# Kernel tuning notes

Measured on AMD Instinct MI355X. Metric: run time of the kernel, lower is better.

Reference implementation:

```python
import jax, jax.numpy as jnp
import numpy as np

D_IN = 1024
D_OUT = 1024
SEQ = 4096


def setup_inputs() -> dict:
    key = jax.random.key(0)
    kx, kq, kk, kv = jax.random.split(key, 4)
    x = jax.random.normal(kx, (SEQ, D_IN), dtype=jnp.float32)
    # original uses torch.rand (uniform [0,1)) for parameter init
    w_query = jax.random.uniform(kq, (D_IN, D_OUT), dtype=jnp.float32)
    w_key = jax.random.uniform(kk, (D_IN, D_OUT), dtype=jnp.float32)
    w_value = jax.random.uniform(kv, (D_IN, D_OUT), dtype=jnp.float32)
    return {"x": x, "w_query": w_query, "w_key": w_key, "w_value": w_value}


def reference(x, w_query, w_key, w_value):
    # QKV projections: [S, d_in] @ [d_in, d_out] -> [S, d_out]
    queries = x @ w_query
    keys = x @ w_key
    values = x @ w_value
    scale = keys.shape[-1] ** 0.5
    # full attention matrix [S, S]
    attn_scores = jnp.einsum('sd,td->st', queries, keys)
    attn_weights = jax.nn.softmax(attn_scores / scale, axis=-1)
    context_vecs = attn_weights @ values  # [S, d_out]
    return context_vecs
```

## Files before the change

kernel.cpp:

```cpp
#include <hip/hip_runtime.h>
#include <hip/hip_fp16.h>
#include <math.h>

#define SEQ    4096
#define DMODEL 1024

typedef _Float16 half8   __attribute__((ext_vector_type(8)));
typedef _Float16 half4v  __attribute__((ext_vector_type(4)));
typedef float    floatx4 __attribute__((ext_vector_type(4)));

__device__ inline void split_val(float v, _Float16& h, _Float16& l) {
    _Float16 hh = (_Float16)v;
    h = hh;
    l = (_Float16)(v - (float)hh);
}

__global__ __launch_bounds__(256) void prep(const float* __restrict__ x,
                                            const float* __restrict__ wq,
                                            const float* __restrict__ wk,
                                            const float* __restrict__ wv,
                                            _Float16* __restrict__ x_hi,
                                            _Float16* __restrict__ x_lo,
                                            _Float16* __restrict__ wqkT_hi,
                                            _Float16* __restrict__ wqkT_lo,
                                            _Float16* __restrict__ wvT) {
    __shared__ float tile[32][33];
    const int b = blockIdx.x;
    if (b < 3072) {
        const int which = b >> 10;
        const int bb = b & 1023;
        const int c0 = (bb & 31) * 32;
        const int r0 = (bb >> 5) * 32;
        const float* w = (which == 0) ? wq : (which == 1) ? wk : wv;
        const int tx = threadIdx.x & 31, ty = threadIdx.x >> 5;
#pragma unroll
        for (int j = 0; j < 4; ++j)
            tile[ty * 4 + j][tx] = w[(size_t)(r0 + ty * 4 + j) * DMODEL + c0 + tx];
        __syncthreads();
        if (which < 2) {
            _Float16* th = wqkT_hi + (size_t)which * DMODEL * DMODEL;
            _Float16* tl = wqkT_lo + (size_t)which * DMODEL * DMODEL;
#pragma unroll
            for (int j = 0; j < 4; ++j) {
                float v = tile[tx][ty * 4 + j];
                size_t idx = (size_t)(c0 + ty * 4 + j) * DMODEL + r0 + tx;
                _Float16 h, l;
                split_val(v, h, l);
                th[idx] = h;
                tl[idx] = l;
            }
        } else {
#pragma unroll
            for (int j = 0; j < 4; ++j)
                wvT[(size_t)(c0 + ty * 4 + j) * DMODEL + r0 + tx] =
                    (_Float16)tile[tx][ty * 4 + j];
        }
    } else {
        const int t0 = (b - 3072) * 256 + threadIdx.x;
#pragma unroll
        for (int rep = 0; rep < 4; ++rep) {
            const size_t i = (size_t)t0 + (size_t)rep * 262144;
            floatx4 v = *(const floatx4*)(x + 4 * i);
            half4v h, l;
#pragma unroll
            for (int j = 0; j < 4; ++j) {
                _Float16 hh = (_Float16)v[j];
                _Float16 ll = (_Float16)(v[j] - (float)hh);
                h[j] = hh;
                l[j] = ll;
            }
            *(half4v*)(x_hi + 4 * i) = h;
            *(half4v*)(x_lo + 4 * i) = l;
        }
    }
}

__global__ __launch_bounds__(512, 1) void gemm_qkproj_dp(
    const _Float16* __restrict__ Ahi, const _Float16* __restrict__ Alo,
    const _Float16* __restrict__ Bhi, const _Float16* __restrict__ Blo,
    _Float16* __restrict__ Qh, _Float16* __restrict__ Kh) {
    __shared__ _Float16 As[4][128][32];
    __shared__ _Float16 Bs[4][256][32];

    const int tid  = threadIdx.x;
    const int lane = tid & 63;
    const int wid  = tid >> 6;
    const int wm   = (wid >> 2) * 64;
    const int wn   = (wid & 3) * 64;

    const int rowA0 = blockIdx.y * 128;
    const int colB0 = blockIdx.x * 256;

    const int ar  = tid >> 2;
    const int ag  = tid & 3;
    const int ags = ag ^ ((ar >> 1) & 3);
    const char* aHiB = (const char*)(Ahi + (size_t)(rowA0 + ar) * DMODEL) + ags * 16;
    const char* aLoB = (const char*)(Alo + (size_t)(rowA0 + ar) * DMODEL) + ags * 16;
    const int br  = tid >> 2;
    const int bg  = tid & 3;
    const int bgs = bg ^ ((br >> 1) & 3);
    const char* bHi0 = (const char*)(Bhi + (size_t)(colB0 + br) * DMODEL) + bgs * 16;
    const char* bHi1 = (const char*)(Bhi + (size_t)(colB0 + br + 128) * DMODEL) + bgs * 16;
    const char* bLo0 = (const char*)(Blo + (size_t)(colB0 + br) * DMODEL) + bgs * 16;
    const char* bLo1 = (const char*)(Blo + (size_t)(colB0 + br + 128) * DMODEL) + bgs * 16;

#define STAGE_QA(tt)                                                                 \
    do {                                                                             \
        const int _s = (tt) & 3;                                                     \
        const char* _ab = ((tt) < 64) ? aHiB : aLoB;                                 \
        const size_t _ko = (size_t)((tt) & 31) * 64;                                 \
        __builtin_amdgcn_global_load_lds(                                            \
            (const __attribute__((address_space(1))) void*)(_ab + _ko),              \
            (__attribute__((address_space(3))) void*)&As[_s][ar][ag * 8], 16, 0, 0); \
    } while (0)

#define STAGE_QB(tt)                                                                 \
    do {                                                                             \
        const int _s = (tt) & 3;                                                     \
        const bool _lo = ((tt) >= 32) && ((tt) < 64);                                \
        const char* _b0 = _lo ? bLo0 : bHi0;                                         \
        const char* _b1 = _lo ? bLo1 : bHi1;                                         \
        const size_t _ko = (size_t)((tt) & 31) * 64;                                 \
        __builtin_amdgcn_global_load_lds(                                            \
            (const __attribute__((address_space(1))) void*)(_b0 + _ko),              \
            (__attribute__((address_space(3))) void*)&Bs[_s][br][bg * 8], 16, 0, 0); \
        __builtin_amdgcn_global_load_lds(                                            \
            (const __attribute__((address_space(1))) void*)(_b1 + _ko),              \
            (__attribute__((address_space(3))) void*)&Bs[_s][br + 128][bg * 8], 16, 0, 0);\
    } while (0)

    const int fm = lane & 15;
    const int fq = lane >> 4;
    const int ck = (fq ^ ((fm >> 1) & 3)) * 8;

    floatx4 acc[4][4] = {};

    auto tile_body = [&](int t, bool do_stage) {
        const int s = t & 3;
        half8 av[4], bv[4];
#pragma unroll
        for (int i = 0; i < 4; ++i) av[i] = *(const half8*)&As[s][wm + i * 16 + fm][ck];
#pragma unroll
        for (int j = 0; j < 4; ++j) bv[j] = *(const half8*)&Bs[s][wn + j * 16 + fm][ck];
        if (do_stage) { STAGE_QA(t + 3); STAGE_QB(t + 3); }
        asm volatile("" ::: "memory");
        __builtin_amdgcn_s_barrier();
        asm volatile("" ::: "memory");
        __builtin_amdgcn_s_setprio(1);
#pragma unroll
        for (int i = 0; i < 4; ++i)
#pragma unroll
            for (int j = 0; j < 4; ++j)
                acc[i][j] = __builtin_amdgcn_mfma_f32_16x16x32_f16(av[i], bv[j], acc[i][j], 0, 0, 0);
        __builtin_amdgcn_s_setprio(0);
    };

    STAGE_QA(0); STAGE_QB(0);
    STAGE_QA(1); STAGE_QB(1);
    STAGE_QA(2); STAGE_QB(2);
    asm volatile("s_waitcnt vmcnt(6)" ::: "memory");
    __builtin_amdgcn_s_barrier();
    asm volatile("" ::: "memory");

#pragma unroll 1
    for (int t = 0; t < 93; ++t) {
        tile_body(t, true);
        asm volatile("s_waitcnt vmcnt(6)" ::: "memory");
        __builtin_amdgcn_s_barrier();
        asm volatile("" ::: "memory");
    }
    tile_body(93, false);
    asm volatile("s_waitcnt vmcnt(3)" ::: "memory");
    __builtin_amdgcn_s_barrier();
    asm volatile("" ::: "memory");
    tile_body(94, false);
    asm volatile("s_waitcnt vmcnt(0)" ::: "memory");
    __builtin_amdgcn_s_barrier();
    asm volatile("" ::: "memory");
    tile_body(95, false);
#undef STAGE_QA
#undef STAGE_QB

    _Float16* dst = Qh;
    int cbase = colB0;
    if (colB0 >= 1024) { dst = Kh; cbase = colB0 - 1024; }

#pragma unroll
    for (int i = 0; i < 4; ++i) {
        const int growb = rowA0 + wm + i * 16 + fq * 4;
#pragma unroll
        for (int j = 0; j < 4; ++j) {
            const int gcol = wn + j * 16 + fm;
#pragma unroll
            for (int r = 0; r < 4; ++r)
                dst[(size_t)(growb + r) * DMODEL + cbase + gcol] =
                    (_Float16)acc[i][j][r];
        }
    }
}

__global__ __launch_bounds__(512, 2) void gemm_score_dp(
    const _Float16* __restrict__ Qh,
    const _Float16* __restrict__ Kh,
    _Float16* __restrict__ Ph, float* __restrict__ Marr, float* __restrict__ Larr,
    float scale) {
    __shared__ _Float16 As[4][256][32];
    __shared__ _Float16 Bs[4][256][32];

    const int tid  = threadIdx.x;
    const int lane = tid & 63;
    const int wid  = tid >> 6;
    const int wm   = (wid >> 2) * 128;
    const int wn   = (wid & 3) * 64;

    const int lin = blockIdx.y * 16 + blockIdx.x;
    const int swz = (lin & 7) * 32 + (lin >> 3);
    const int rowA0 = (swz >> 4) * 256;
    const int colB0 = (swz & 15) * 256;

    const int pr  = tid >> 2;
    const int pg  = tid & 3;
    const int pgs = pg ^ ((pr >> 1) & 3);

    const char* aSrc0 = (const char*)(Qh + (size_t)(rowA0 + pr) * DMODEL) + pgs * 16;
    const char* aSrc1 = (const char*)(Qh + (size_t)(rowA0 + pr + 128) * DMODEL) + pgs * 16;
    const char* bSrc0 = (const char*)(Kh + (size_t)(colB0 + pr) * DMODEL) + pgs * 16;
    const char* bSrc1 = (const char*)(Kh + (size_t)(colB0 + pr + 128) * DMODEL) + pgs * 16;

#define STAGE_A(t)                                                                  \
    do {                                                                            \
        const int _s = (t) & 3;                                                     \
        const size_t _ko = (size_t)(t) * 64;                                        \
        __builtin_amdgcn_global_load_lds(                                           \
            (const __attribute__((address_space(1))) void*)(aSrc0 + _ko),           \
            (__attribute__((address_space(3))) void*)&As[_s][pr][pg * 8], 16, 0, 0);\
        __builtin_amdgcn_global_load_lds(                                           \
            (const __attribute__((address_space(1))) void*)(aSrc1 + _ko),           \
            (__attribute__((address_space(3))) void*)&As[_s][pr + 128][pg * 8], 16, 0, 0);\
    } while (0)

#define STAGE_B(t)                                                                  \
    do {                                                                            \
        const int _s = (t) & 3;                                                     \
        const size_t _ko = (size_t)(t) * 64;                                        \
        __builtin_amdgcn_global_load_lds(                                           \
            (const __attribute__((address_space(1))) void*)(bSrc0 + _ko),           \
            (__attribute__((address_space(3))) void*)&Bs[_s][pr][pg * 8], 16, 0, 0);\
        __builtin_amdgcn_global_load_lds(                                           \
            (const __attribute__((address_space(1))) void*)(bSrc1 + _ko),           \
            (__attribute__((address_space(3))) void*)&Bs[_s][pr + 128][pg * 8], 16, 0, 0);\
    } while (0)

    const int fm = lane & 15;
    const int fq = lane >> 4;
    const int ck = (fq ^ ((fm >> 1) & 3)) * 8;

    floatx4 acc[8][4] = {};

    auto tile_body = [&](int t, bool do_stage) {
        const int s = t & 3;
        half8 av[4], av2[4], bv[4];
#pragma unroll
        for (int i = 0; i < 4; ++i) av[i]  = *(const half8*)&As[s][wm + i * 16 + fm][ck];
#pragma unroll
        for (int i = 0; i < 4; ++i) av2[i] = *(const half8*)&As[s][wm + 64 + i * 16 + fm][ck];
#pragma unroll
        for (int j = 0; j < 4; ++j) bv[j]  = *(const half8*)&Bs[s][wn + j * 16 + fm][ck];
        if (do_stage) { STAGE_A(t + 3); STAGE_B(t + 3); }
        asm volatile("" ::: "memory");
        __builtin_amdgcn_s_barrier();
        asm volatile("" ::: "memory");
        __builtin_amdgcn_s_setprio(1);
#pragma unroll
        for (int i = 0; i < 4; ++i)
#pragma unroll
            for (int j = 0; j < 4; ++j)
                acc[i][j] = __builtin_amdgcn_mfma_f32_16x16x32_f16(av[i], bv[j], acc[i][j], 0, 0, 0);
#pragma unroll
        for (int i = 0; i < 4; ++i)
#pragma unroll
            for (int j = 0; j < 4; ++j)
                acc[i + 4][j] = __builtin_amdgcn_mfma_f32_16x16x32_f16(av2[i], bv[j], acc[i + 4][j], 0, 0, 0);
        __builtin_amdgcn_s_setprio(0);
    };

    STAGE_A(0); STAGE_B(0);
    STAGE_A(1); STAGE_B(1);
    STAGE_A(2); STAGE_B(2);
    asm volatile("s_waitcnt vmcnt(8)" ::: "memory");
    __builtin_amdgcn_s_barrier();
    asm volatile("" ::: "memory");

#pragma unroll 1
    for (int t = 0; t < 29; ++t) {
        tile_body(t, true);
        asm volatile("s_waitcnt vmcnt(8)" ::: "memory");
        __builtin_amdgcn_s_barrier();
        asm volatile("" ::: "memory");
    }
    tile_body(29, false);
    asm volatile("s_waitcnt vmcnt(4)" ::: "memory");
    __builtin_amdgcn_s_barrier();
    asm volatile("" ::: "memory");
    tile_body(30, false);
    asm volatile("s_waitcnt vmcnt(0)" ::: "memory");
    __builtin_amdgcn_s_barrier();
    asm volatile("" ::: "memory");
    tile_body(31, false);
#undef STAGE_A
#undef STAGE_B

    const int tprime = (colB0 + wn) >> 6;
#pragma unroll
    for (int i = 0; i < 8; ++i) {
#pragma unroll
        for (int r = 0; r < 4; ++r) {
            const int grow = rowA0 + wm + i * 16 + fq * 4 + r;
            float s0 = acc[i][0][r] * scale;
            float s1 = acc[i][1][r] * scale;
            float s2 = acc[i][2][r] * scale;
            float s3 = acc[i][3][r] * scale;
            float mx = fmaxf(fmaxf(s0, s1), fmaxf(s2, s3));
            mx = fmaxf(mx, __shfl_xor(mx, 1));
            mx = fmaxf(mx, __shfl_xor(mx, 2));
            mx = fmaxf(mx, __shfl_xor(mx, 4));
            mx = fmaxf(mx, __shfl_xor(mx, 8));
            float p0 = __expf(s0 - mx);
            float p1 = __expf(s1 - mx);
            float p2 = __expf(s2 - mx);
            float p3 = __expf(s3 - mx);
            float sum = p0 + p1 + p2 + p3;
            sum += __shfl_xor(sum, 1);
            sum += __shfl_xor(sum, 2);
            sum += __shfl_xor(sum, 4);
            sum += __shfl_xor(sum, 8);
            _Float16* prow = Ph + (size_t)grow * SEQ + colB0 + wn + fm;
            prow[0]  = (_Float16)p0;
            prow[16] = (_Float16)p1;
            prow[32] = (_Float16)p2;
            prow[48] = (_Float16)p3;
            if (fm == 0) {
                Marr[(size_t)grow * 64 + tprime] = mx;
                Larr[(size_t)grow * 64 + tprime] = sum;
            }
        }
    }
}

__global__ __launch_bounds__(256) void compute_c(const float* __restrict__ Marr,
                                                 const float* __restrict__ Larr,
                                                 _Float16* __restrict__ CarrT) {
    __shared__ float c_s[64][65];
    const int row0 = blockIdx.x * 64;
    const int wv = threadIdx.x >> 6;
    const int ln = threadIdx.x & 63;

#pragma unroll
    for (int k = 0; k < 16; ++k) {
        const int r = wv * 16 + k;
        float mt = Marr[(size_t)(row0 + r) * 64 + ln];
        float lt = Larr[(size_t)(row0 + r) * 64 + ln];
        float m = mt;
#pragma unroll
        for (int off = 32; off > 0; off >>= 1) m = fmaxf(m, __shfl_xor(m, off));
        float e = __expf(mt - m);
        float L = lt * e;
#pragma unroll
        for (int off = 32; off > 0; off >>= 1) L += __shfl_xor(L, off);
        c_s[r][ln] = e / L;
    }
    __syncthreads();

#pragma unroll
    for (int k = 0; k < 16; ++k) {
        const int t = wv * 16 + k;
        CarrT[(size_t)t * SEQ + row0 + ln] = (_Float16)c_s[ln][t];
    }
}

__global__ __launch_bounds__(512, 1) void gemm_pv_dp(
    const _Float16* __restrict__ P,
    const _Float16* __restrict__ VT,
    const _Float16* __restrict__ CarrT,
    float* __restrict__ out) {
    __shared__ _Float16 As[4][128][64];
    __shared__ _Float16 Bs[4][128][64];
    __shared__ _Float16 cT[64][128];

    const int tid  = threadIdx.x;
    const int lane = tid & 63;
    const int wid  = tid >> 6;
    const int wm   = (wid >> 2) * 64;
    const int wn   = (wid & 3) * 32;

    const int rowA0 = blockIdx.y * 128;
    const int colB0 = blockIdx.x * 128;

    {
        int g = tid;
#pragma unroll
        for (int it = 0; it < 2; ++it, g += 512) {
            const int t  = g >> 4;
            const int r8 = (g & 15) * 8;
            *(half8*)&cT[t][r8] =
                *(const half8*)(CarrT + (size_t)t * SEQ + rowA0 + r8);
        }
    }
    __syncthreads();

    const int prow = tid >> 3;
    const int pgr  = tid & 7;
    const int ags  = pgr ^ (prow & 7);
    const char* aSrc0 = (const char*)(P  + (size_t)(rowA0 + prow) * SEQ) + ags * 16;
    const char* aSrc1 = (const char*)(P  + (size_t)(rowA0 + prow + 64) * SEQ) + ags * 16;
    const char* bSrc0 = (const char*)(VT + (size_t)(colB0 + prow) * SEQ) + ags * 16;
    const char* bSrc1 = (const char*)(VT + (size_t)(colB0 + prow + 64) * SEQ) + ags * 16;

#define STAGE_PA(tt)                                                                \
    do {                                                                            \
        const int _s = (tt) & 3;                                                    \
        const size_t _ko = (size_t)(tt) * 128;                                      \
        __builtin_amdgcn_global_load_lds(                                           \
            (const __attribute__((address_space(1))) void*)(aSrc0 + _ko),           \
            (__attribute__((address_space(3))) void*)&As[_s][prow][pgr * 8], 16, 0, 0);\
        __builtin_amdgcn_global_load_lds(                                           \
            (const __attribute__((address_space(1))) void*)(aSrc1 + _ko),           \
            (__attribute__((address_space(3))) void*)&As[_s][prow + 64][pgr * 8], 16, 0, 0);\
    } while (0)

#define STAGE_PB(tt)                                                                \
    do {                                                                            \
        const int _s = (tt) & 3;                                                    \
        const size_t _ko = (size_t)(tt) * 128;                                      \
        __builtin_amdgcn_global_load_lds(                                           \
            (const __attribute__((address_space(1))) void*)(bSrc0 + _ko),           \
            (__attribute__((address_space(3))) void*)&Bs[_s][prow][pgr * 8], 16, 0, 0);\
        __builtin_amdgcn_global_load_lds(                                           \
            (const __attribute__((address_space(1))) void*)(bSrc1 + _ko),           \
            (__attribute__((address_space(3))) void*)&Bs[_s][prow + 64][pgr * 8], 16, 0, 0);\
    } while (0)

    const int fm = lane & 15;
    const int fq = lane >> 4;
    const int ck0 = ((fq    ) ^ (fm & 7)) * 8;
    const int ck1 = ((fq + 4) ^ (fm & 7)) * 8;

    floatx4 acc[4][2] = {};

    auto tile_body = [&](int t, bool do_stage) {
        const int s = t & 3;
        half8 av[4], av2[4], bv[2], bv2[2];
        _Float16 cs[4];
#pragma unroll
        for (int i = 0; i < 4; ++i) {
            av[i]  = *(const half8*)&As[s][wm + i * 16 + fm][ck0];
            av2[i] = *(const half8*)&As[s][wm + i * 16 + fm][ck1];
            cs[i]  = cT[t][wm + i * 16 + fm];
        }
#pragma unroll
        for (int j = 0; j < 2; ++j) {
            bv[j]  = *(const half8*)&Bs[s][wn + j * 16 + fm][ck0];
            bv2[j] = *(const half8*)&Bs[s][wn + j * 16 + fm][ck1];
        }
#pragma unroll
        for (int i = 0; i < 4; ++i)
#pragma unroll
            for (int e = 0; e < 8; ++e) {
                av[i][e]  *= cs[i];
                av2[i][e] *= cs[i];
            }
        if (do_stage) { STAGE_PA(t + 3); STAGE_PB(t + 3); }
        asm volatile("" ::: "memory");
        __builtin_amdgcn_s_barrier();
        asm volatile("" ::: "memory");
        __builtin_amdgcn_s_setprio(1);
#pragma unroll
        for (int i = 0; i < 4; ++i)
#pragma unroll
            for (int j = 0; j < 2; ++j)
                acc[i][j] = __builtin_amdgcn_mfma_f32_16x16x32_f16(av[i], bv[j], acc[i][j], 0, 0, 0);
#pragma unroll
        for (int i = 0; i < 4; ++i)
#pragma unroll
            for (int j = 0; j < 2; ++j)
                acc[i][j] = __builtin_amdgcn_mfma_f32_16x16x32_f16(av2[i], bv2[j], acc[i][j], 0, 0, 0);
        __builtin_amdgcn_s_setprio(0);
    };

    STAGE_PA(0); STAGE_PB(0);
    STAGE_PA(1); STAGE_PB(1);
    STAGE_PA(2); STAGE_PB(2);
    asm volatile("s_waitcnt vmcnt(8)" ::: "memory");
    __builtin_amdgcn_s_barrier();
    asm volatile("" ::: "memory");

#pragma unroll 1
    for (int t = 0; t < 61; ++t) {
        tile_body(t, true);
        asm volatile("s_waitcnt vmcnt(8)" ::: "memory");
        __builtin_amdgcn_s_barrier();
        asm volatile("" ::: "memory");
    }
    tile_body(61, false);
    asm volatile("s_waitcnt vmcnt(4)" ::: "memory");
    __builtin_amdgcn_s_barrier();
    asm volatile("" ::: "memory");
    tile_body(62, false);
    asm volatile("s_waitcnt vmcnt(0)" ::: "memory");
    __builtin_amdgcn_s_barrier();
    asm volatile("" ::: "memory");
    tile_body(63, false);
#undef STAGE_PA
#undef STAGE_PB

#pragma unroll
    for (int i = 0; i < 4; ++i) {
        const int growb = rowA0 + wm + i * 16 + fq * 4;
#pragma unroll
        for (int j = 0; j < 2; ++j) {
            const int gcol = colB0 + wn + j * 16 + fm;
#pragma unroll
            for (int r = 0; r < 4; ++r)
                out[(size_t)(growb + r) * DMODEL + gcol] = acc[i][j][r];
        }
    }
}

template <int OUT_HALF>
__global__ __launch_bounds__(256) void gemm_h16_n64(
    const _Float16* __restrict__ A, int lda,
    const _Float16* __restrict__ B, int ldb,
    float* __restrict__ Cf, _Float16* __restrict__ Ch,
    int N, int K) {
    __shared__ _Float16 Ah[128][32];
    __shared__ _Float16 Bh[64][32];

    const int tid = threadIdx.x;
    const int lane = tid & 63;
    const int w = tid >> 6;
    const int wm = (w >> 1) * 64;
    const int wn = (w & 1) * 32;

    const int rowA0 = blockIdx.y * 128;
    const int colB0 = blockIdx.x * 64;

    const int sr = lane >> 2;
    const int sc = lane & 3;
    const int ra0 = w * 32 + sr;
    const int ra1 = ra0 + 16;
    const int rb0 = w * 16 + sr;
    const int cga0 = sc ^ ((ra0 >> 1) & 3);
    const int cga1 = sc ^ ((ra1 >> 1) & 3);
    const int cgb0 = sc ^ ((rb0 >> 1) & 3);

    const char* gp[3];
    gp[0] = (const char*)(A + (size_t)(rowA0 + ra0) * lda) + cga0 * 16;
    gp[1] = (const char*)(A + (size_t)(rowA0 + ra1) * lda) + cga1 * 16;
    gp[2] = (const char*)(B + (size_t)(colB0 + rb0) * ldb) + cgb0 * 16;

    _Float16* lp[3] = {
        &Ah[w * 32][0], &Ah[w * 32 + 16][0],
        &Bh[w * 16][0],
    };

    const int fm = lane & 15;
    const int fq = lane >> 4;
    const int ck = ((fq ^ ((fm >> 1) & 3)) * 8);

    floatx4 acc[4][2] = {};

    for (int k0 = 0; k0 < K; k0 += 32) {
#pragma unroll
        for (int t = 0; t < 3; ++t)
            __builtin_amdgcn_global_load_lds(
                (const __attribute__((address_space(1))) void*)gp[t],
                (__attribute__((address_space(3))) void*)lp[t], 16, 0, 0);
#pragma unroll
        for (int t = 0; t < 3; ++t) gp[t] += 64;
        __syncthreads();

        half8 av[4], bv[2];
#pragma unroll
        for (int i = 0; i < 4; ++i)
            av[i] = *(const half8*)&Ah[wm + i * 16 + fm][ck];
#pragma unroll
        for (int j = 0; j < 2; ++j)
            bv[j] = *(const half8*)&Bh[wn + j * 16 + fm][ck];
#pragma unroll
        for (int i = 0; i < 4; ++i)
#pragma unroll
            for (int j = 0; j < 2; ++j)
                acc[i][j] = __builtin_amdgcn_mfma_f32_16x16x32_f16(av[i], bv[j], acc[i][j], 0, 0, 0);
        __syncthreads();
    }

#pragma unroll
    for (int i = 0; i < 4; ++i) {
        const int growb = rowA0 + wm + i * 16 + fq * 4;
#pragma unroll
        for (int j = 0; j < 2; ++j) {
            const int gcol = colB0 + wn + j * 16 + fm;
#pragma unroll
            for (int r = 0; r < 4; ++r) {
                float v = acc[i][j][r];
                size_t idx = (size_t)(growb + r) * N + gcol;
                if (OUT_HALF) Ch[idx] = (_Float16)v;
                else          Cf[idx] = v;
            }
        }
    }
}

extern "C" void kernel_launch(void* const* d_in, const int* in_sizes, int n_in,
                              void* d_out, int out_size, void* d_ws, size_t ws_size,
                              hipStream_t stream) {
    const float* x  = (const float*)d_in[0];
    const float* wq = (const float*)d_in[1];
    const float* wk = (const float*)d_in[2];
    const float* wv = (const float*)d_in[3];
    float* out = (float*)d_out;

    char* base = (char*)d_ws;
    const size_t MB = 1u << 20;
    _Float16* P       = (_Float16*)base;
    _Float16* x_hi    = (_Float16*)(base + 0 * MB);
    _Float16* x_lo    = (_Float16*)(base + 8 * MB);
    _Float16* wqkT_hi = (_Float16*)(base + 16 * MB);
    _Float16* wqkT_lo = (_Float16*)(base + 20 * MB);
    _Float16* wvT     = (_Float16*)(base + 24 * MB);
    float*    Marr    = (float*)(base + 32 * MB);
    float*    Larr    = (float*)(base + 33 * MB);
    _Float16* CarrT   = (_Float16*)(base + 34 * MB);
    _Float16* Qh      = (_Float16*)(base + 64 * MB);
    _Float16* Kh      = (_Float16*)(base + 72 * MB);
    _Float16* VT      = (_Float16*)(base + 96 * MB);

    prep<<<4096, 256, 0, stream>>>(x, wq, wk, wv, x_hi, x_lo, wqkT_hi, wqkT_lo, wvT);

    dim3 gqk(2048 / 256, SEQ / 128);
    gemm_qkproj_dp<<<gqk, dim3(512), 0, stream>>>(x_hi, x_lo, wqkT_hi, wqkT_lo,
                                                  Qh, Kh);
    dim3 gvt(SEQ / 64, DMODEL / 128);
    gemm_h16_n64<1><<<gvt, 256, 0, stream>>>(wvT, DMODEL, x_hi, DMODEL,
                                             nullptr, VT, SEQ, DMODEL);

    dim3 gs(SEQ / 256, SEQ / 256);
    gemm_score_dp<<<gs, dim3(512), 0, stream>>>(Qh, Kh, P, Marr, Larr,
                                                1.0f / 32.0f);

    compute_c<<<SEQ / 64, 256, 0, stream>>>(Marr, Larr, CarrT);

    dim3 gpv(DMODEL / 128, SEQ / 128);
    gemm_pv_dp<<<gpv, dim3(512), 0, stream>>>(P, VT, CarrT, out);
}
```

Baseline: 262.2 us.

## Stage hi and lo split tiles together to reuse A/B fragments across MFMAs

```diff
diff --git a/kernel.cpp b/kernel.cpp
--- a/kernel.cpp
+++ b/kernel.cpp
@@ -79,8 +79,10 @@
     const _Float16* __restrict__ Ahi, const _Float16* __restrict__ Alo,
     const _Float16* __restrict__ Bhi, const _Float16* __restrict__ Blo,
     _Float16* __restrict__ Qh, _Float16* __restrict__ Kh) {
-    __shared__ _Float16 As[4][128][32];
-    __shared__ _Float16 Bs[4][256][32];
+    __shared__ _Float16 Ah[3][128][32];
+    __shared__ _Float16 Al[3][128][32];
+    __shared__ _Float16 Bh[3][256][32];
+    __shared__ _Float16 Bl[3][256][32];
 
     const int tid  = threadIdx.x;
     const int lane = tid & 63;
@@ -94,39 +96,35 @@
     const int ar  = tid >> 2;
     const int ag  = tid & 3;
     const int ags = ag ^ ((ar >> 1) & 3);
-    const char* aHiB = (const char*)(Ahi + (size_t)(rowA0 + ar) * DMODEL) + ags * 16;
-    const char* aLoB = (const char*)(Alo + (size_t)(rowA0 + ar) * DMODEL) + ags * 16;
-    const int br  = tid >> 2;
-    const int bg  = tid & 3;
-    const int bgs = bg ^ ((br >> 1) & 3);
-    const char* bHi0 = (const char*)(Bhi + (size_t)(colB0 + br) * DMODEL) + bgs * 16;
-    const char* bHi1 = (const char*)(Bhi + (size_t)(colB0 + br + 128) * DMODEL) + bgs * 16;
-    const char* bLo0 = (const char*)(Blo + (size_t)(colB0 + br) * DMODEL) + bgs * 16;
-    const char* bLo1 = (const char*)(Blo + (size_t)(colB0 + br + 128) * DMODEL) + bgs * 16;
-
-#define STAGE_QA(tt)                                                                 \
+    const char* aHiS = (const char*)(Ahi + (size_t)(rowA0 + ar) * DMODEL) + ags * 16;
+    const char* aLoS = (const char*)(Alo + (size_t)(rowA0 + ar) * DMODEL) + ags * 16;
+    const char* bHi0 = (const char*)(Bhi + (size_t)(colB0 + ar) * DMODEL) + ags * 16;
+    const char* bHi1 = (const char*)(Bhi + (size_t)(colB0 + ar + 128) * DMODEL) + ags * 16;
+    const char* bLo0 = (const char*)(Blo + (size_t)(colB0 + ar) * DMODEL) + ags * 16;
+    const char* bLo1 = (const char*)(Blo + (size_t)(colB0 + ar + 128) * DMODEL) + ags * 16;
+
+#define STAGE_Q(tt)                                                                  \
     do {                                                                             \
-        const int _s = (tt) & 3;                                                     \
-        const char* _ab = ((tt) < 64) ? aHiB : aLoB;                                 \
-        const size_t _ko = (size_t)((tt) & 31) * 64;                                 \
+        const int _s = (tt) % 3;                                                     \
+        const size_t _ko = (size_t)(tt) * 64;                                        \
         __builtin_amdgcn_global_load_lds(                                            \
-            (const __attribute__((address_space(1))) void*)(_ab + _ko),              \
-            (__attribute__((address_space(3))) void*)&As[_s][ar][ag * 8], 16, 0, 0); \
-    } while (0)
-
-#define STAGE_QB(tt)                                                                 \
-    do {                                                                             \
-        const int _s = (tt) & 3;                                                     \
-        const bool _lo = ((tt) >= 32) && ((tt) < 64);                                \
-        const char* _b0 = _lo ? bLo0 : bHi0;                                         \
-        const char* _b1 = _lo ? bLo1 : bHi1;                                         \
-        const size_t _ko = (size_t)((tt) & 31) * 64;                                 \
+            (const __attribute__((address_space(1))) void*)(aHiS + _ko),             \
+            (__attribute__((address_space(3))) void*)&Ah[_s][ar][ag * 8], 16, 0, 0); \
         __builtin_amdgcn_global_load_lds(                                            \
-            (const __attribute__((address_space(1))) void*)(_b0 + _ko),              \
-            (__attribute__((address_space(3))) void*)&Bs[_s][br][bg * 8], 16, 0, 0); \
+            (const __attribute__((address_space(1))) void*)(aLoS + _ko),             \
+            (__attribute__((address_space(3))) void*)&Al[_s][ar][ag * 8], 16, 0, 0); \
         __builtin_amdgcn_global_load_lds(                                            \
-            (const __attribute__((address_space(1))) void*)(_b1 + _ko),              \
-            (__attribute__((address_space(3))) void*)&Bs[_s][br + 128][bg * 8], 16, 0, 0);\
+            (const __attribute__((address_space(1))) void*)(bHi0 + _ko),             \
+            (__attribute__((address_space(3))) void*)&Bh[_s][ar][ag * 8], 16, 0, 0); \
+        __builtin_amdgcn_global_load_lds(                                            \
+            (const __attribute__((address_space(1))) void*)(bHi1 + _ko),             \
+            (__attribute__((address_space(3))) void*)&Bh[_s][ar + 128][ag * 8], 16, 0, 0);\
+        __builtin_amdgcn_global_load_lds(                                            \
+            (const __attribute__((address_space(1))) void*)(bLo0 + _ko),             \
+            (__attribute__((address_space(3))) void*)&Bl[_s][ar][ag * 8], 16, 0, 0); \
+        __builtin_amdgcn_global_load_lds(                                            \
+            (const __attribute__((address_space(1))) void*)(bLo1 + _ko),             \
+            (__attribute__((address_space(3))) void*)&Bl[_s][ar + 128][ag * 8], 16, 0, 0);\
     } while (0)
 
     const int fm = lane & 15;
@@ -136,13 +134,19 @@
     floatx4 acc[4][4] = {};
 
     auto tile_body = [&](int t, bool do_stage) {
-        const int s = t & 3;
-        half8 av[4], bv[4];
-#pragma unroll
-        for (int i = 0; i < 4; ++i) av[i] = *(const half8*)&As[s][wm + i * 16 + fm][ck];
-#pragma unroll
-        for (int j = 0; j < 4; ++j) bv[j] = *(const half8*)&Bs[s][wn + j * 16 + fm][ck];
-        if (do_stage) { STAGE_QA(t + 3); STAGE_QB(t + 3); }
+        const int s = t % 3;
+        half8 avh[4], avl[4], bvh[4], bvl[4];
+#pragma unroll
+        for (int i = 0; i < 4; ++i) {
+            avh[i] = *(const half8*)&Ah[s][wm + i * 16 + fm][ck];
+            avl[i] = *(const half8*)&Al[s][wm + i * 16 + fm][ck];
+        }
+#pragma unroll
+        for (int j = 0; j < 4; ++j) {
+            bvh[j] = *(const half8*)&Bh[s][wn + j * 16 + fm][ck];
+            bvl[j] = *(const half8*)&Bl[s][wn + j * 16 + fm][ck];
+        }
+        if (do_stage) STAGE_Q(t + 2);
         asm volatile("" ::: "memory");
         __builtin_amdgcn_s_barrier();
         asm volatile("" ::: "memory");
@@ -151,35 +155,39 @@
         for (int i = 0; i < 4; ++i)
 #pragma unroll
             for (int j = 0; j < 4; ++j)
-                acc[i][j] = __builtin_amdgcn_mfma_f32_16x16x32_f16(av[i], bv[j], acc[i][j], 0, 0, 0);
+                acc[i][j] = __builtin_amdgcn_mfma_f32_16x16x32_f16(avh[i], bvh[j], acc[i][j], 0, 0, 0);
+#pragma unroll
+        for (int i = 0; i < 4; ++i)
+#pragma unroll
+            for (int j = 0; j < 4; ++j)
+                acc[i][j] = __builtin_amdgcn_mfma_f32_16x16x32_f16(avh[i], bvl[j], acc[i][j], 0, 0, 0);
+#pragma unroll
+        for (int i = 0; i < 4; ++i)
+#pragma unroll
+            for (int j = 0; j < 4; ++j)
+                acc[i][j] = __builtin_amdgcn_mfma_f32_16x16x32_f16(avl[i], bvh[j], acc[i][j], 0, 0, 0);
         __builtin_amdgcn_s_setprio(0);
     };
 
-    STAGE_QA(0); STAGE_QB(0);
-    STAGE_QA(1); STAGE_QB(1);
-    STAGE_QA(2); STAGE_QB(2);
+    STAGE_Q(0);
+    STAGE_Q(1);
     asm volatile("s_waitcnt vmcnt(6)" ::: "memory");
     __builtin_amdgcn_s_barrier();
     asm volatile("" ::: "memory");
 
 #pragma unroll 1
-    for (int t = 0; t < 93; ++t) {
+    for (int t = 0; t < 30; ++t) {
         tile_body(t, true);
         asm volatile("s_waitcnt vmcnt(6)" ::: "memory");
         __builtin_amdgcn_s_barrier();
         asm volatile("" ::: "memory");
     }
-    tile_body(93, false);
-    asm volatile("s_waitcnt vmcnt(3)" ::: "memory");
-    __builtin_amdgcn_s_barrier();
-    asm volatile("" ::: "memory");
-    tile_body(94, false);
+    tile_body(30, false);
     asm volatile("s_waitcnt vmcnt(0)" ::: "memory");
     __builtin_amdgcn_s_barrier();
     asm volatile("" ::: "memory");
-    tile_body(95, false);
-#undef STAGE_QA
-#undef STAGE_QB
+    tile_body(31, false);
+#undef STAGE_Q
 
     _Float16* dst = Qh;
     int cbase = colB0;
```

After: 252.1 us. 3.9% less time.
